# Kernel optimization log

Measured on AMD Instinct MI355X. Metric: run time of the kernel, lower is better.

Reference implementation:

```python
import jax, jax.numpy as jnp
import numpy as np

B, N, S, K = 16, 4096, 1024, 32
DIN, DINC, DOUT = 64, 67, 64
MAX_VALUE = 1e10


def setup_inputs() -> dict:
    key = jax.random.key(0)
    ks = jax.random.split(key, 6)
    x = jax.random.normal(ks[0], (B, N, DIN), dtype=jnp.float32)
    x_complete = jax.random.normal(ks[1], (B, N, DINC), dtype=jnp.float32)
    # neighbor indices in [-1, N); -1 denotes padding (masked out in pooling)
    indexes = jax.random.randint(ks[2], (B, S, K), -1, N, dtype=jnp.int64)
    # first neighbor is the center point and must be valid
    indexes = indexes.at[:, :, 0].set(jnp.abs(indexes[:, :, 0]) % N)
    weight1 = jax.random.normal(ks[3], (DOUT, DINC), dtype=jnp.float32) * 0.05
    weight2 = jax.random.normal(ks[4], (DOUT, DIN), dtype=jnp.float32) * 0.05
    bias = jax.random.normal(ks[5], (DOUT,), dtype=jnp.float32) * 0.05
    return {"x": x, "x_complete": x_complete, "indexes": indexes,
            "weight1": weight1, "weight2": weight2, "bias": bias, "use_x": 1}


def reference(x, x_complete, indexes, weight1, weight2, bias, use_x):
    # pooling_operation = 'max' (hardcoded; string arg in original module)
    Bq, Nq, _ = x.shape
    _, Sq, Kq = indexes.shape
    C = weight1.shape[0]
    # dense linear projections
    xc = jnp.einsum('bnd,cd->bnc', x_complete, weight1) + bias  # (B,N,C)
    xp = jnp.einsum('bnd,cd->bnc', x, weight2)                  # (B,N,C)
    if use_x:
        xc = xc + xp
    # prepend a zero row so index -1 (-> slot 0) gathers zeros
    pad = jnp.concatenate([jnp.zeros((Bq, 1, C), xc.dtype), xc], axis=1)  # (B,N+1,C)
    idx1 = indexes + 1                                          # (B,S,K)
    g = jnp.take_along_axis(pad, idx1.reshape(Bq, Sq * Kq, 1), axis=1)
    g = g.reshape(Bq, Sq, Kq, C)                                # (B,S,K,C)
    if use_x:
        if Nq == Sq:
            g = g - xp[:, :, None, :]
        else:
            xp_pad = jnp.concatenate([jnp.zeros((Bq, 1, C), xp.dtype), xp], axis=1)
            center = jnp.take_along_axis(xp_pad, (indexes[:, :, 0] + 1)[:, :, None], axis=1)  # (B,S,C)
            g = g - center[:, :, None, :]
    # masked max over the neighbor axis: padded slots pushed to -MAX_VALUE
    mask = (idx1 == 0).astype(g.dtype)[..., None]               # (B,S,K,1)
    out = jnp.max(g - MAX_VALUE * mask, axis=2)                 # (B,S,C)
    return out
```

## Files before the change

### kernel.cpp

```cpp
#include <hip/hip_runtime.h>

#define B_    16
#define N_    4096
#define S_    1024
#define K_    32
#define DIN_  64
#define DINC_ 67
#define DOUT_ 64
#define ROWS_ (B_ * N_)
#define NCH   128
#define NP1   (N_ + 1)
#define NTILE 28
#define ASTR  168
#define WLDSB (NTILE * 64 * 16)
#define ALDSB (64 * ASTR * 2)

typedef float f32x4 __attribute__((ext_vector_type(4)));
typedef short s16x8 __attribute__((ext_vector_type(8)));

static __device__ __forceinline__ unsigned short f2bf(float f) {
    unsigned int u = __float_as_uint(f);
    u = (u + 0x7fffu + ((u >> 16) & 1u)) >> 16;
    return (unsigned short)u;
}
static __device__ __forceinline__ float bf2f(unsigned short h) {
    return __uint_as_float((unsigned int)h << 16);
}
static __device__ __forceinline__ unsigned int pack2(float a, float b) {
    return (unsigned int)f2bf(a) | ((unsigned int)f2bf(b) << 16);
}

__global__ __launch_bounds__(256) void proj_kernel(
    const float* __restrict__ x, const float* __restrict__ xcm,
    const float* __restrict__ w1, const float* __restrict__ w2,
    const float* __restrict__ bias, const int* __restrict__ use_x_p,
    unsigned short* __restrict__ cmb)
{
    __shared__ char smem[WLDSB + ALDSB];
    uint4* ldsb          = (uint4*)smem;
    unsigned short* lwb  = (unsigned short*)smem;
    unsigned short* lact = (unsigned short*)(smem + WLDSB);
    unsigned int*  ldsd  = (unsigned int*)lact;

    const int t    = threadIdx.x;
    const int row0 = (blockIdx.x & 7) * (ROWS_ / 8) + (blockIdx.x >> 3) * 64;
    const int ux   = use_x_p[0];
    const int bb   = row0 >> 12;

    if ((row0 & (N_ - 1)) == 0 && t < 16) {
        uint4* sp = (uint4*)(cmb + (size_t)bb * NP1 * NCH);
        sp[t] = (t < 8)
            ? make_uint4(0xff80ff80u, 0xff80ff80u, 0xff80ff80u, 0xff80ff80u)
            : make_uint4(0u, 0u, 0u, 0u);
    }

    ldsb[1536 + t] = make_uint4(0u, 0u, 0u, 0u);
    __syncthreads();

#pragma unroll
    for (int it = 0; it < 2; ++it) {
        const int wid = it * 256 + t;
        const int c   = wid >> 3, kc = wid & 7;
        const int s   = kc >> 2,  q  = kc & 3;
        const float4 v0 = *(const float4*)(w2 + c * DIN_ + kc * 8);
        const float4 v1 = *(const float4*)(w2 + c * DIN_ + kc * 8 + 4);
        uint4 pk;
        pk.x = pack2(v0.x, v0.y); pk.y = pack2(v0.z, v0.w);
        pk.z = pack2(v1.x, v1.y); pk.w = pack2(v1.z, v1.w);
        const int lane = q * 16 + (c & 15);
        ldsb[(s * 8 + 4 + (c >> 4)) * 64 + lane] = pk;
        ldsb[(s * 8 + (c >> 4)) * 64 + lane] =
            ux ? pk : make_uint4(0u, 0u, 0u, 0u);
    }

#pragma unroll
    for (int it = 0; it < 2; ++it) {
        const int wid = it * 256 + t;
        const int t16 = wid >> 6;
        const int l   = wid & 63;
        const int q   = l >> 4, m = l & 15;
        const int c   = (t16 & 3) * 16 + m;
        const int db  = ((t16 >> 2) << 5) + q * 8;
        const float* wp = w1 + c * DINC_ + db;
        const float4 v0 = *(const float4*)(wp);
        const float4 v1 = *(const float4*)(wp + 4);
        uint4 pk;
        pk.x = pack2(v0.x, v0.y); pk.y = pack2(v0.z, v0.w);
        pk.z = pack2(v1.x, v1.y); pk.w = pack2(v1.z, v1.w);
        ldsb[(16 + t16) * 64 + l] = pk;
    }
    if (t < 64) {
        const int c     = t;
        const int chunk = (24 + (t >> 4)) * 64 + (t & 15);
        const float* wr = w1 + c * DINC_ + 64;
        lwb[chunk * 8 + 0] = f2bf(wr[0]);
        lwb[chunk * 8 + 1] = f2bf(wr[1]);
        lwb[chunk * 8 + 2] = f2bf(wr[2]);
    }

    {
        const float4* sx4 = (const float4*)(x + (size_t)row0 * DIN_);
#pragma unroll
        for (int j = 0; j < 4; ++j) {
            const int idx = j * 256 + t;
            const float4 v = sx4[idx];
            const int row = idx >> 4, f4 = idx & 15;
            *(uint2*)(ldsd + row * 84 + f4 * 2) =
                make_uint2(pack2(v.x, v.y), pack2(v.z, v.w));
        }
    }
#pragma unroll
    for (int it = 0; it < 2; ++it) {
        const int wid = it * 256 + t;
        const int row = wid >> 3, dg = wid & 7;
        const float* sp = xcm + (size_t)(row0 + row) * DINC_ + dg * 8;
        const float4 v0 = *(const float4*)(sp);
        const float4 v1 = *(const float4*)(sp + 4);
        uint4 pk;
        pk.x = pack2(v0.x, v0.y); pk.y = pack2(v0.z, v0.w);
        pk.z = pack2(v1.x, v1.y); pk.w = pack2(v1.z, v1.w);
        *(uint4*)(lact + row * ASTR + 64 + dg * 8) = pk;
    }
    if (t < 64) {
        const float* sp = xcm + (size_t)(row0 + t) * DINC_ + 64;
        unsigned short* dp = lact + t * ASTR + 128;
        dp[0] = f2bf(sp[0]); dp[1] = f2bf(sp[1]); dp[2] = f2bf(sp[2]); dp[3] = 0;
    }
    for (int i = t; i < 64 * 14; i += 256) {
        const int row = i / 14, j2 = i - row * 14;
        ldsd[row * 84 + 66 + j2] = 0;
    }
    __syncthreads();

    const int l = t & 63;
    const int w = __builtin_amdgcn_readfirstlane(t >> 6);
    const int q = l >> 4, m = l & 15;

    const unsigned short* arow = lact + (w * 16 + m) * ASTR;
    s16x8 af[5];
#pragma unroll
    for (int s = 0; s < 5; ++s)
        af[s] = *(const s16x8*)(arow + s * 32 + q * 8);

    const s16x8* bfr = (const s16x8*)ldsb;

    f32x4 acc[8];
#pragma unroll
    for (int nt = 0; nt < 8; ++nt) acc[nt] = (f32x4){0.f, 0.f, 0.f, 0.f};

#pragma unroll
    for (int s = 0; s < 2; ++s)
#pragma unroll
        for (int nt = 0; nt < 8; ++nt)
            acc[nt] = __builtin_amdgcn_mfma_f32_16x16x32_bf16(
                bfr[(s * 8 + nt) * 64 + l], af[s], acc[nt], 0, 0, 0);
#pragma unroll
    for (int s = 2; s < 5; ++s)
#pragma unroll
        for (int nt = 0; nt < 4; ++nt)
            acc[nt] = __builtin_amdgcn_mfma_f32_16x16x32_bf16(
                bfr[(16 + (s - 2) * 4 + nt) * 64 + l], af[s], acc[nt], 0, 0, 0);

    const int row_g = row0 + w * 16 + m;
    unsigned short* rowp = cmb + (size_t)(row_g + bb + 1) * NCH;
    const int chq = q * 4;
#pragma unroll
    for (int nt = 0; nt < 8; ++nt) {
        f32x4 a = acc[nt];
        if (nt < 4) {
            const float4 bv = *(const float4*)(bias + nt * 16 + chq);
            a[0] += bv.x; a[1] += bv.y; a[2] += bv.z; a[3] += bv.w;
        }
        *(uint2*)(rowp + nt * 16 + chq) =
            make_uint2(pack2(a[0], a[1]), pack2(a[2], a[3]));
    }
}

__global__ __launch_bounds__(256) void gather_max_kernel(
    const int* __restrict__ indexes, const unsigned short* __restrict__ cmb,
    const int* __restrict__ use_x_p, float* __restrict__ out)
{
    const int lane = threadIdx.x & 63;
    const int h    = lane >> 5;
    const int ln   = lane & 31;
    const int wv   = __builtin_amdgcn_readfirstlane(threadIdx.x >> 6);
    const int grp  = (blockIdx.x & 7) * 1024 + (blockIdx.x >> 3) * 4 + wv;
    const int pairA = grp * 2;
    const int b     = grp >> 9;
    const int ux    = use_x_p[0];

    const int* iA = indexes + (size_t)pairA * K_;
    const int* iB = iA + K_;
    const char* cb = (const char*)cmb + (size_t)b * NP1 * 256;
    const unsigned lnoff = (unsigned)(ln << 2);

    const float NEG = -__builtin_inff();
    float m0 = NEG, m1 = NEG;
#pragma unroll
    for (int k = 0; k < K_; ++k) {
        const int ik = h ? iB[k] : iA[k];
        const unsigned off = ((unsigned)(ik + 1) << 8) + lnoff;
        const unsigned int v = *(const unsigned int*)(cb + off);
        m0 = fmaxf(m0, bf2f((unsigned short)(v & 0xffff)));
        m1 = fmaxf(m1, bf2f((unsigned short)(v >> 16)));
    }
    if (ux) {
        const int i0 = h ? iB[0] : iA[0];
        const unsigned off0 = ((unsigned)(i0 + 1) << 8) + 128u + lnoff;
        const unsigned int c = *(const unsigned int*)(cb + off0);
        m0 -= bf2f((unsigned short)(c & 0xffff));
        m1 -= bf2f((unsigned short)(c >> 16));
    }
    const int pair = pairA + h;
    *(float2*)(out + (size_t)pair * 64 + ln * 2) = make_float2(m0, m1);
}

__global__ __launch_bounds__(256, 1) void fused_fallback_kernel(
    const float* __restrict__ x, const float* __restrict__ xcm,
    const int* __restrict__ indexes,
    const float* __restrict__ w1, const float* __restrict__ w2,
    const float* __restrict__ bias, const int* __restrict__ use_x_p,
    float* __restrict__ out)
{
    const int lane = threadIdx.x & 63;
    const int pair = (blockIdx.x * blockDim.x + threadIdx.x) >> 6;
    const int b    = pair >> 10;
    const int ux   = use_x_p[0];

    float W1[DINC_];
#pragma unroll
    for (int j = 0; j < DINC_; ++j) W1[j] = w1[lane * DINC_ + j];
    float W2[DIN_];
#pragma unroll
    for (int j = 0; j < DIN_; ++j) W2[j] = w2[lane * DIN_ + j];
    const float bv = bias[lane];

    const int* idxp  = indexes + (size_t)pair * K_;
    const int  myidx = idxp[lane & 31];

    const float NEG = -__builtin_inff();
    float m = NEG;
    for (int k = 0; k < K_; ++k) {
        const int ik = __shfl(myidx, k, 64);
        if (ik < 0) continue;
        const float* xc_row = xcm + ((size_t)b * N_ + ik) * DINC_;
        float a1 = bv;
#pragma unroll
        for (int j = 0; j < DINC_; ++j) a1 += xc_row[j] * W1[j];
        if (ux) {
            const float* x_row = x + ((size_t)b * N_ + ik) * DIN_;
            float a2 = 0.f;
#pragma unroll
            for (int j = 0; j < DIN_; ++j) a2 += x_row[j] * W2[j];
            a1 += a2;
        }
        m = fmaxf(m, a1);
    }
    if (ux) {
        const int i0 = __shfl(myidx, 0, 64);
        const float* x_row = x + ((size_t)b * N_ + i0) * DIN_;
        float a2 = 0.f;
#pragma unroll
        for (int j = 0; j < DIN_; ++j) a2 += x_row[j] * W2[j];
        m -= a2;
    }
    out[(size_t)pair * DOUT_ + lane] = m;
}

extern "C" void kernel_launch(void* const* d_in, const int* in_sizes, int n_in,
                              void* d_out, int out_size, void* d_ws, size_t ws_size,
                              hipStream_t stream)
{
    const float* x    = (const float*)d_in[0];
    const float* xcm  = (const float*)d_in[1];
    const int*   idx  = (const int*)d_in[2];
    const float* w1   = (const float*)d_in[3];
    const float* w2   = (const float*)d_in[4];
    const float* bias = (const float*)d_in[5];
    const int*   ux   = (const int*)d_in[6];
    float* out = (float*)d_out;

    const size_t cmb_bytes =
        (size_t)(ROWS_ + B_) * NCH * sizeof(unsigned short);
    const int npairs = B_ * S_;

    if (ws_size >= cmb_bytes) {
        unsigned short* cmb = (unsigned short*)d_ws;
        proj_kernel<<<ROWS_ / 64, 256, 0, stream>>>(x, xcm, w1, w2, bias, ux, cmb);
        gather_max_kernel<<<(npairs / 2) / 4, 256, 0, stream>>>(idx, cmb, ux, out);
    } else {
        fused_fallback_kernel<<<npairs / 4, 256, 0, stream>>>(x, xcm, idx, w1, w2,
                                                              bias, ux, out);
    }
}
```

Before: 100.5 us.

## Widen gather loads to 16 bytes per lane with 8 pairs per wave

Restructures the gather-max kernel so each lane handles 8 channels of one pair through a 16-byte load, with 8 lanes per pair and 8 pairs per wave. The lane's full index row is preloaded with int4 loads, replacing the per-k scalar index reads. The grid shrinks from 2048 to 512 blocks. The aim is fewer, wider memory instructions and more independent gathers in flight, at the cost of extra registers, lower occupancy from the smaller grid, and index reads that are no longer uniform across the wave.

```diff
diff --git a/kernel.cpp b/kernel.cpp
--- a/kernel.cpp
+++ b/kernel.cpp
@@ -29,6 +29,12 @@
 static __device__ __forceinline__ unsigned int pack2(float a, float b) {
     return (unsigned int)f2bf(a) | ((unsigned int)f2bf(b) << 16);
 }
+static __device__ __forceinline__ float bflo(unsigned int u) {
+    return __uint_as_float(u << 16);
+}
+static __device__ __forceinline__ float bfhi(unsigned int u) {
+    return __uint_as_float(u & 0xffff0000u);
+}
 
 __global__ __launch_bounds__(256) void proj_kernel(
     const float* __restrict__ x, const float* __restrict__ xcm,
@@ -181,38 +187,50 @@
     const int* __restrict__ use_x_p, float* __restrict__ out)
 {
     const int lane = threadIdx.x & 63;
-    const int h    = lane >> 5;
-    const int ln   = lane & 31;
     const int wv   = __builtin_amdgcn_readfirstlane(threadIdx.x >> 6);
-    const int grp  = (blockIdx.x & 7) * 1024 + (blockIdx.x >> 3) * 4 + wv;
-    const int pairA = grp * 2;
-    const int b     = grp >> 9;
-    const int ux    = use_x_p[0];
-
-    const int* iA = indexes + (size_t)pairA * K_;
-    const int* iB = iA + K_;
+    const int pairBase = (blockIdx.x & 7) * 2048 + (blockIdx.x >> 3) * 32 + wv * 8;
+    const int pair = pairBase + (lane >> 3);
+    const int o    = lane & 7;
+    const int b    = pairBase >> 10;
+    const int ux   = use_x_p[0];
+
     const char* cb = (const char*)cmb + (size_t)b * NP1 * 256;
-    const unsigned lnoff = (unsigned)(ln << 2);
+    const unsigned chb = (unsigned)(o << 4);
+
+    const int* ip = indexes + (size_t)pair * K_;
+    int idxr[32];
+#pragma unroll
+    for (int kb = 0; kb < 8; ++kb) {
+        const int4 v = *(const int4*)(ip + kb * 4);
+        idxr[kb * 4 + 0] = v.x; idxr[kb * 4 + 1] = v.y;
+        idxr[kb * 4 + 2] = v.z; idxr[kb * 4 + 3] = v.w;
+    }
 
     const float NEG = -__builtin_inff();
-    float m0 = NEG, m1 = NEG;
+    float m[8];
+#pragma unroll
+    for (int j = 0; j < 8; ++j) m[j] = NEG;
+
 #pragma unroll
     for (int k = 0; k < K_; ++k) {
-        const int ik = h ? iB[k] : iA[k];
-        const unsigned off = ((unsigned)(ik + 1) << 8) + lnoff;
-        const unsigned int v = *(const unsigned int*)(cb + off);
-        m0 = fmaxf(m0, bf2f((unsigned short)(v & 0xffff)));
-        m1 = fmaxf(m1, bf2f((unsigned short)(v >> 16)));
+        const unsigned off = ((unsigned)(idxr[k] + 1) << 8) + chb;
+        const uint4 v = *(const uint4*)(cb + off);
+        m[0] = fmaxf(m[0], bflo(v.x)); m[1] = fmaxf(m[1], bfhi(v.x));
+        m[2] = fmaxf(m[2], bflo(v.y)); m[3] = fmaxf(m[3], bfhi(v.y));
+        m[4] = fmaxf(m[4], bflo(v.z)); m[5] = fmaxf(m[5], bfhi(v.z));
+        m[6] = fmaxf(m[6], bflo(v.w)); m[7] = fmaxf(m[7], bfhi(v.w));
     }
     if (ux) {
-        const int i0 = h ? iB[0] : iA[0];
-        const unsigned off0 = ((unsigned)(i0 + 1) << 8) + 128u + lnoff;
-        const unsigned int c = *(const unsigned int*)(cb + off0);
-        m0 -= bf2f((unsigned short)(c & 0xffff));
-        m1 -= bf2f((unsigned short)(c >> 16));
-    }
-    const int pair = pairA + h;
-    *(float2*)(out + (size_t)pair * 64 + ln * 2) = make_float2(m0, m1);
+        const unsigned off0 = ((unsigned)(idxr[0] + 1) << 8) + 128u + chb;
+        const uint4 c = *(const uint4*)(cb + off0);
+        m[0] -= bflo(c.x); m[1] -= bfhi(c.x);
+        m[2] -= bflo(c.y); m[3] -= bfhi(c.y);
+        m[4] -= bflo(c.z); m[5] -= bfhi(c.z);
+        m[6] -= bflo(c.w); m[7] -= bfhi(c.w);
+    }
+    float* op = out + (size_t)pair * DOUT_ + o * 8;
+    *(float4*)op       = make_float4(m[0], m[1], m[2], m[3]);
+    *(float4*)(op + 4) = make_float4(m[4], m[5], m[6], m[7]);
 }
 
 __global__ __launch_bounds__(256, 1) void fused_fallback_kernel(
@@ -287,7 +305,7 @@
     if (ws_size >= cmb_bytes) {
         unsigned short* cmb = (unsigned short*)d_ws;
         proj_kernel<<<ROWS_ / 64, 256, 0, stream>>>(x, xcm, w1, w2, bias, ux, cmb);
-        gather_max_kernel<<<(npairs / 2) / 4, 256, 0, stream>>>(idx, cmb, ux, out);
+        gather_max_kernel<<<512, 256, 0, stream>>>(idx, cmb, ux, out);
     } else {
         fused_fallback_kernel<<<npairs / 4, 256, 0, stream>>>(x, xcm, idx, w1, w2,
                                                               bias, ux, out);
```

Measured after the change: 98.96 us. No clear change (-1.5%).
